# Optimization experiments

Hardware: AMD Instinct MI355X
Metric: run time of the kernel (lower is better)

## Reference

```python
import jax, jax.numpy as jnp
import numpy as np

N = 100000   # nodes
E = 1600000  # edges (avg degree 16)
D = 128      # emb_dim
L = 5        # num_layer
NUM_BOND_TYPE = 6
NUM_ATOM_TYPE = 120
EPS = 1e-5


def setup_inputs() -> dict:
    key = jax.random.key(0)
    ks = jax.random.split(key, 10)
    s = 0.05
    x = jax.random.randint(ks[0], (N, 2), 0, 3)
    edge_index = jax.random.randint(ks[1], (2, E), 0, N)
    edge_attr = jax.random.randint(ks[2], (E, 2), 0, 3)
    # learned params: x embedding table [120+3, D], per-layer edge tables [6+3, D], GIN MLPs, BN stats
    x_emb = jax.random.normal(ks[3], (123, D), dtype=jnp.float32) * s
    etab = jax.random.normal(ks[4], (L, 9, D), dtype=jnp.float32) * s
    w1 = jax.random.normal(ks[5], (L, 2 * D, D), dtype=jnp.float32) * s
    b1 = jnp.zeros((L, 2 * D), dtype=jnp.float32)
    w2 = jax.random.normal(ks[6], (L, D, 2 * D), dtype=jnp.float32) * s
    b2 = jnp.zeros((L, D), dtype=jnp.float32)
    gamma = jnp.ones((L, D), dtype=jnp.float32)
    beta = jnp.zeros((L, D), dtype=jnp.float32)
    bn_mean = jax.random.normal(ks[7], (L, D), dtype=jnp.float32) * 0.1
    bn_var = jax.random.uniform(ks[8], (L, D), minval=0.5, maxval=1.5, dtype=jnp.float32)
    return dict(x=x, edge_index=edge_index, edge_attr=edge_attr, x_emb=x_emb, etab=etab,
                w1=w1, b1=b1, w2=w2, b2=b2, gamma=gamma, beta=beta,
                bn_mean=bn_mean, bn_var=bn_var)


def reference(x, edge_index, edge_attr, x_emb, etab, w1, b1, w2, b2, gamma, beta, bn_mean, bn_var):
    # node input embedding: atom-type rows [0:120) + chirality rows [120:123)
    h = x_emb[:NUM_ATOM_TYPE][x[:, 0]] + x_emb[NUM_ATOM_TYPE:][x[:, 1]]  # [N, D]
    # add self-loops (self-loop attr = (bond_type=4, direction=0))
    loop = jnp.arange(N, dtype=edge_index.dtype)
    src = jnp.concatenate([edge_index[0], loop])  # [E+N]
    dst = jnp.concatenate([edge_index[1], loop])  # [E+N]
    eb = jnp.concatenate([edge_attr[:, 0], jnp.full((N,), 4, dtype=edge_attr.dtype)])
    ed = jnp.concatenate([edge_attr[:, 1], jnp.zeros((N,), dtype=edge_attr.dtype)])
    for l in range(L):
        # edge embedding: bond-type rows [0:6) + direction rows [6:9)
        e = etab[l][:NUM_BOND_TYPE][eb] + etab[l][NUM_BOND_TYPE:][ed]  # [E+N, D]
        msg = h[src] + e                                               # gather + add
        agg = jax.ops.segment_sum(msg, dst, num_segments=N)           # scatter-add aggregate
        # GIN MLP: Linear(D,2D) -> ReLU -> Linear(2D,D)  (torch Linear: y = x @ W.T + b)
        hmid = jax.nn.relu(jnp.einsum('nd,hd->nh', agg, w1[l]) + b1[l])
        h2 = jnp.einsum('nh,dh->nd', hmid, w2[l]) + b2[l]
        # BatchNorm1d (eval mode, running stats)
        h2 = (h2 - bn_mean[l]) * jax.lax.rsqrt(bn_var[l] + EPS) * gamma[l] + beta[l]
        h = jax.nn.relu(h2) if l < L - 1 else h2  # JK='last', dropout p=0
    return h
```

## Files before the change

kernel.cpp:

```cpp
#include <hip/hip_runtime.h>

#define D 128
#define H 256
#define NBLK 512
#define BUCKSH 8

typedef _Float16 half8 __attribute__((ext_vector_type(8)));
typedef _Float16 half4 __attribute__((ext_vector_type(4)));
typedef _Float16 half2v __attribute__((ext_vector_type(2)));
typedef float floatx4 __attribute__((ext_vector_type(4)));
typedef float floatx2 __attribute__((ext_vector_type(2)));

__device__ inline unsigned char f32_to_fp8(float v){
  int p = __builtin_amdgcn_cvt_pk_fp8_f32(v, v, 0, false);
  return (unsigned char)(p & 0xFF);
}

__global__ __launch_bounds__(256) void scan_part(const int* __restrict__ cnt,
                                                 int* __restrict__ bsum, int N){
  int base = blockIdx.x*1024;
  int tid = threadIdx.x;
  int idx = base + tid*4;
  int4 v = {0,0,0,0};
  if (idx + 3 < N) v = *(const int4*)(cnt + idx);
  else {
    if (idx   < N) v.x = cnt[idx];
    if (idx+1 < N) v.y = cnt[idx+1];
    if (idx+2 < N) v.z = cnt[idx+2];
    if (idx+3 < N) v.w = cnt[idx+3];
  }
  int s = v.x + v.y + v.z + v.w;
  #pragma unroll
  for (int off = 32; off > 0; off >>= 1) s += __shfl_down(s, off, 64);
  __shared__ int ws[4];
  int lane = tid & 63, wave = tid >> 6;
  if (lane == 0) ws[wave] = s;
  __syncthreads();
  if (tid == 0) bsum[blockIdx.x] = ws[0] + ws[1] + ws[2] + ws[3];
}

__global__ __launch_bounds__(1024) void scan_bsums(const int* __restrict__ bsum,
                                                   int* __restrict__ bbase,
                                                   int* __restrict__ total_out, int nb, int N){
  __shared__ int sh[1024];
  int tid = threadIdx.x;
  int v = (tid < nb) ? bsum[tid] : 0;
  sh[tid] = v;
  __syncthreads();
  #pragma unroll
  for (int off = 1; off < 1024; off <<= 1){
    int t = 0;
    if (tid >= off) t = sh[tid - off];
    __syncthreads();
    if (tid >= off) sh[tid] += t;
    __syncthreads();
  }
  if (tid < nb) bbase[tid] = sh[tid] - v;
  if (tid == 0) total_out[N] = sh[1023];
}

__global__ __launch_bounds__(256) void scan_emit(const int* __restrict__ cnt,
                                                 const int* __restrict__ bbase,
                                                 int* __restrict__ outp, int N){
  int base = blockIdx.x*1024;
  int tid = threadIdx.x;
  int idx = base + tid*4;
  int4 v = {0,0,0,0};
  if (idx + 3 < N) v = *(const int4*)(cnt + idx);
  else {
    if (idx   < N) v.x = cnt[idx];
    if (idx+1 < N) v.y = cnt[idx+1];
    if (idx+2 < N) v.z = cnt[idx+2];
    if (idx+3 < N) v.w = cnt[idx+3];
  }
  int s = v.x + v.y + v.z + v.w;
  int lane = tid & 63, wave = tid >> 6;
  int incl = s;
  #pragma unroll
  for (int off = 1; off < 64; off <<= 1){
    int t = __shfl_up(incl, off, 64);
    if (lane >= off) incl += t;
  }
  __shared__ int ws[4];
  if (lane == 63) ws[wave] = incl;
  __syncthreads();
  int woff = 0;
  #pragma unroll
  for (int w = 0; w < 4; ++w) if (w < wave) woff += ws[w];
  int off0 = bbase[blockIdx.x] + woff + (incl - s);
  if (idx   < N) outp[idx]   = off0;
  if (idx+1 < N) outp[idx+1] = off0 + v.x;
  if (idx+2 < N) outp[idx+2] = off0 + v.x + v.y;
  if (idx+3 < N) outp[idx+3] = off0 + v.x + v.y + v.z;
}

__global__ __launch_bounds__(256) void part_count(const int* __restrict__ dst,
                                                  int* __restrict__ cntBB,
                                                  int E, int chunk, int nbuck){
  __shared__ int lc[512];
  int b = blockIdx.x;
  for (int i = threadIdx.x; i < nbuck; i += 256) lc[i] = 0;
  __syncthreads();
  int e0 = b*chunk, e1 = min(e0 + chunk, E);
  for (int e = e0 + threadIdx.x; e < e1; e += 256)
    atomicAdd(&lc[dst[e] >> BUCKSH], 1);
  __syncthreads();
  for (int i = threadIdx.x; i < nbuck; i += 256) cntBB[i*NBLK + b] = lc[i];
}

__global__ __launch_bounds__(256) void part_bin(const int* __restrict__ src,
                                                const int* __restrict__ dst,
                                                const int* __restrict__ ea,
                                                const int* __restrict__ baseBB,
                                                unsigned* __restrict__ staged,
                                                int E, int chunk, int nbuck){
  __shared__ int run[512];
  int b = blockIdx.x;
  for (int i = threadIdx.x; i < nbuck; i += 256) run[i] = baseBB[i*NBLK + b];
  __syncthreads();
  int e0 = b*chunk, e1 = min(e0 + chunk, E);
  for (int e = e0 + threadIdx.x; e < e1; e += 256){
    int d = dst[e];
    unsigned pv = ((unsigned)(d & 255) << 24) |
                  ((unsigned)(ea[2*e]*3 + ea[2*e+1]) << 20) | (unsigned)src[e];
    int pos = atomicAdd(&run[d >> BUCKSH], 1);
    staged[pos] = pv;
  }
}

__global__ __launch_bounds__(256) void part_emit(const unsigned* __restrict__ staged,
                                                 const int* __restrict__ baseBB,
                                                 unsigned* __restrict__ packed,
                                                 int* __restrict__ rowptr,
                                                 int N, int E, int nbuck, int M){
  __shared__ int ncnt[256];
  __shared__ int sscan[256];
  __shared__ int basep[256];
  __shared__ int cur[256];
  int k = blockIdx.x;
  int tid = threadIdx.x;
  int bstart = baseBB[k*NBLK];
  int bend = (k+1 < nbuck) ? baseBB[(k+1)*NBLK] : baseBB[M];
  ncnt[tid] = 0; cur[tid] = 0;
  __syncthreads();
  for (int j = bstart + tid; j < bend; j += 256)
    atomicAdd(&ncnt[staged[j] >> 24], 1);
  __syncthreads();
  int v = ncnt[tid];
  sscan[tid] = v;
  __syncthreads();
  #pragma unroll
  for (int off = 1; off < 256; off <<= 1){
    int t = (tid >= off) ? sscan[tid-off] : 0;
    __syncthreads();
    sscan[tid] += t;
    __syncthreads();
  }
  int excl = sscan[tid] - v;
  basep[tid] = bstart + excl;
  int node = k*256 + tid;
  if (node < N) rowptr[node] = bstart + excl;
  if (k == nbuck-1 && tid == 0) rowptr[N] = E;
  __syncthreads();
  for (int j = bstart + tid; j < bend; j += 256){
    unsigned s = staged[j];
    int dloc = (int)(s >> 24);
    int pos = basep[dloc] + atomicAdd(&cur[dloc], 1);
    packed[pos] = s & 0xFFFFFFu;
  }
}

__global__ void embed_kernel(const int* __restrict__ x, const float* __restrict__ xemb,
                             unsigned char* __restrict__ h, int N){
  int t = blockIdx.x*256 + threadIdx.x;
  if (t >= N*16) return;
  int n = t >> 4, c = (t & 15) * 8;
  int x0 = x[2*n], x1 = x[2*n+1];
  const float* r0 = xemb + (size_t)x0*D + c;
  const float* r1 = xemb + (size_t)(120 + x1)*D + c;
  float f[8];
  #pragma unroll
  for (int j = 0; j < 8; ++j) f[j] = r0[j] + r1[j];
  int w0 = 0, w1v = 0;
  w0  = __builtin_amdgcn_cvt_pk_fp8_f32(f[0], f[1], w0,  false);
  w0  = __builtin_amdgcn_cvt_pk_fp8_f32(f[2], f[3], w0,  true);
  w1v = __builtin_amdgcn_cvt_pk_fp8_f32(f[4], f[5], w1v, false);
  w1v = __builtin_amdgcn_cvt_pk_fp8_f32(f[6], f[7], w1v, true);
  uint2 o; o.x = (unsigned)w0; o.y = (unsigned)w1v;
  *(uint2*)(h + (size_t)n*D + c) = o;
}

__global__ void prep_tables(const float* __restrict__ etab, const float* __restrict__ gamma,
                            const float* __restrict__ beta, const float* __restrict__ mean,
                            const float* __restrict__ var, const float* __restrict__ b2,
                            float* __restrict__ comb, float* __restrict__ sc, float* __restrict__ sh){
  int l = blockIdx.x, d = threadIdx.x;
  const float* et = etab + (size_t)l*9*D;
  float* cl = comb + (size_t)l*10*D;
  #pragma unroll
  for (int b = 0; b < 3; ++b)
    #pragma unroll
    for (int dd = 0; dd < 3; ++dd)
      cl[(b*3+dd)*D + d] = et[b*D + d] + et[(6+dd)*D + d];
  cl[9*D + d] = et[4*D + d] + et[6*D + d];
  float A = gamma[l*D+d] * rsqrtf(var[l*D+d] + 1e-5f);
  sc[l*D+d] = A;
  sh[l*D+d] = (b2[l*D+d] - mean[l*D+d]) * A + beta[l*D+d];
}

__global__ void repack_weights(const float* __restrict__ w1, const float* __restrict__ w2,
                               _Float16* __restrict__ w1f, _Float16* __restrict__ w2f, int total){
  int i = blockIdx.x*256 + threadIdx.x;
  if (i >= total) return;
  int l = i / (H*D), r = i % (H*D);
  {
    int n = r / D, k = r % D;
    w1f[(size_t)l*H*D + (size_t)(k>>3)*(H*8) + n*8 + (k&7)] = (_Float16)w1[i];
  }
  {
    int n2 = r / H, k2 = r % H;
    w2f[(size_t)l*D*H + (size_t)(k2>>3)*(D*8) + n2*8 + (k2&7)] = (_Float16)w2[i];
  }
}

__global__ __launch_bounds__(256) void agg_kernel(
    const unsigned char* __restrict__ h, const unsigned* __restrict__ packed,
    const int* __restrict__ rowptr, const float* __restrict__ comb,
    _Float16* __restrict__ agg, int N){
  __shared__ float cl[10*D];
  int tid = threadIdx.x;
  for (int i = tid; i < 10*D; i += 256) cl[i] = comb[i];
  __syncthreads();
  int lane = tid & 63;
  int q = lane >> 4, l16 = lane & 15;
  int node = blockIdx.x*16 + (tid >> 6)*4 + q;
  bool valid = node < N;
  int nd = valid ? node : 0;
  int c = l16 * 8;
  float a0, a1, a2, a3, a4, a5, a6, a7;
  {
    uint2 hx = *(const uint2*)(h + (size_t)nd*D + c);
    floatx2 s0 = __builtin_amdgcn_cvt_pk_f32_fp8((int)hx.x, false);
    floatx2 s1 = __builtin_amdgcn_cvt_pk_f32_fp8((int)hx.x, true);
    floatx2 s2 = __builtin_amdgcn_cvt_pk_f32_fp8((int)hx.y, false);
    floatx2 s3 = __builtin_amdgcn_cvt_pk_f32_fp8((int)hx.y, true);
    a0 = s0[0] + cl[9*D + c    ];
    a1 = s0[1] + cl[9*D + c + 1];
    a2 = s1[0] + cl[9*D + c + 2];
    a3 = s1[1] + cl[9*D + c + 3];
    a4 = s2[0] + cl[9*D + c + 4];
    a5 = s2[1] + cl[9*D + c + 5];
    a6 = s3[0] + cl[9*D + c + 6];
    a7 = s3[1] + cl[9*D + c + 7];
  }
  int beg = rowptr[nd], end = rowptr[nd+1];
  unsigned long long cp = 0;
  unsigned p[16], pn[16];
  {
    int m0 = end - beg;
    #pragma unroll
    for (int k = 0; k < 16; ++k) if (k < m0) p[k] = packed[beg+k];
  }
  for (int j = beg; j < end; j += 16){
    int m = end - j;
    uint2 v[16];
    #pragma unroll
    for (int k = 0; k < 16; ++k) if (k < m)
      v[k] = *(const uint2*)(h + (size_t)(p[k] & 0xFFFFFu)*D + c);
    int mn = end - (j + 16);
    #pragma unroll
    for (int k = 0; k < 16; ++k) if (k < mn) pn[k] = packed[j+16+k];
    #pragma unroll
    for (int k = 0; k < 16; ++k) if (k < m){
      cp += 1ULL << (7*(int)(p[k] >> 20));
      floatx2 g0 = __builtin_amdgcn_cvt_pk_f32_fp8((int)v[k].x, false);
      floatx2 g1 = __builtin_amdgcn_cvt_pk_f32_fp8((int)v[k].x, true);
      floatx2 g2 = __builtin_amdgcn_cvt_pk_f32_fp8((int)v[k].y, false);
      floatx2 g3 = __builtin_amdgcn_cvt_pk_f32_fp8((int)v[k].y, true);
      a0 += g0[0]; a1 += g0[1]; a2 += g1[0]; a3 += g1[1];
      a4 += g2[0]; a5 += g2[1]; a6 += g3[0]; a7 += g3[1];
    }
    #pragma unroll
    for (int k = 0; k < 16; ++k) p[k] = pn[k];
  }
  #pragma unroll
  for (int cd = 0; cd < 9; ++cd){
    float cnt = (float)(int)((cp >> (7*cd)) & 127);
    a0 += cnt * cl[cd*D + c    ];
    a1 += cnt * cl[cd*D + c + 1];
    a2 += cnt * cl[cd*D + c + 2];
    a3 += cnt * cl[cd*D + c + 3];
    a4 += cnt * cl[cd*D + c + 4];
    a5 += cnt * cl[cd*D + c + 5];
    a6 += cnt * cl[cd*D + c + 6];
    a7 += cnt * cl[cd*D + c + 7];
  }
  if (valid){
    half8 o;
    o[0] = (_Float16)a0; o[1] = (_Float16)a1;
    o[2] = (_Float16)a2; o[3] = (_Float16)a3;
    o[4] = (_Float16)a4; o[5] = (_Float16)a5;
    o[6] = (_Float16)a6; o[7] = (_Float16)a7;
    *(half8*)(agg + (size_t)node*D + c) = o;
  }
}

__global__ __launch_bounds__(256) void mlp_kernel(
    const _Float16* __restrict__ agg, const _Float16* __restrict__ w1f,
    const _Float16* __restrict__ w2f, const float* __restrict__ b1,
    const float* __restrict__ sc, const float* __restrict__ sh,
    unsigned char* __restrict__ hout, float* __restrict__ fout,
    int N, int relu_out){
  __shared__ __align__(16) char smem[64*256*2];
  _Float16* atile = (_Float16*)smem;
  _Float16* hmid  = (_Float16*)smem;
  int tid = threadIdx.x;
  int wave = tid >> 6, lane = tid & 63;
  int quad = lane >> 4, l15 = lane & 15;
  int r0 = blockIdx.x * 64;

  half8 zf;
  #pragma unroll
  for (int j = 0; j < 8; ++j) zf[j] = (_Float16)0.f;

  #pragma unroll
  for (int i = 0; i < 4; ++i){
    int ci = i*256 + tid;
    int row = ci >> 4, c8 = ci & 15;
    int m = r0 + row;
    half8 v = (m < N) ? *(const half8*)(agg + (size_t)m*D + c8*8) : zf;
    *(half8*)(atile + row*128 + ((c8 ^ (row & 15)) * 8)) = v;
  }
  __syncthreads();

  floatx4 acc[4][4] = {};
  half8 bcur[4], bnxt[4];
  #pragma unroll
  for (int nt = 0; nt < 4; ++nt)
    bcur[nt] = *(const half8*)(w1f + (size_t)quad*(H*8) + (wave*64 + nt*16 + l15)*8);
  #pragma unroll
  for (int ks = 0; ks < 4; ++ks){
    if (ks < 3){
      #pragma unroll
      for (int nt = 0; nt < 4; ++nt)
        bnxt[nt] = *(const half8*)(w1f + (size_t)((ks+1)*4 + quad)*(H*8) + (wave*64 + nt*16 + l15)*8);
    }
    int c8 = ks*4 + quad;
    half8 af[4];
    #pragma unroll
    for (int mt = 0; mt < 4; ++mt)
      af[mt] = *(const half8*)(atile + (mt*16 + l15)*128 + ((c8 ^ l15) * 8));
    #pragma unroll
    for (int mt = 0; mt < 4; ++mt)
      #pragma unroll
      for (int nt = 0; nt < 4; ++nt)
        acc[mt][nt] = __builtin_amdgcn_mfma_f32_16x16x32_f16(af[mt], bcur[nt], acc[mt][nt], 0, 0, 0);
    #pragma unroll
    for (int nt = 0; nt < 4; ++nt) bcur[nt] = bnxt[nt];
  }
  __syncthreads();

  #pragma unroll
  for (int nt = 0; nt < 4; ++nt){
    int n = wave*64 + nt*16 + l15;
    float bias = b1[n];
    #pragma unroll
    for (int mt = 0; mt < 4; ++mt)
      #pragma unroll
      for (int r = 0; r < 4; ++r){
        int row = mt*16 + quad*4 + r;
        hmid[row*256 + (((n >> 3) ^ (row & 31)) * 8) + (n & 7)] =
            (_Float16)fmaxf(acc[mt][nt][r] + bias, 0.f);
      }
  }
  __syncthreads();

  floatx4 acc2[4][2] = {};
  half8 gcur[2], gnxt[2];
  #pragma unroll
  for (int nt = 0; nt < 2; ++nt)
    gcur[nt] = *(const half8*)(w2f + (size_t)quad*(D*8) + (wave*32 + nt*16 + l15)*8);
  #pragma unroll
  for (int ks = 0; ks < 8; ++ks){
    if (ks < 7){
      #pragma unroll
      for (int nt = 0; nt < 2; ++nt)
        gnxt[nt] = *(const half8*)(w2f + (size_t)((ks+1)*4 + quad)*(D*8) + (wave*32 + nt*16 + l15)*8);
    }
    int c8 = ks*4 + quad;
    half8 af[4];
    #pragma unroll
    for (int mt = 0; mt < 4; ++mt){
      int row = mt*16 + l15;
      af[mt] = *(const half8*)(hmid + row*256 + ((c8 ^ (row & 31)) * 8));
    }
    #pragma unroll
    for (int mt = 0; mt < 4; ++mt)
      #pragma unroll
      for (int nt = 0; nt < 2; ++nt)
        acc2[mt][nt] = __builtin_amdgcn_mfma_f32_16x16x32_f16(af[mt], gcur[nt], acc2[mt][nt], 0, 0, 0);
    #pragma unroll
    for (int nt = 0; nt < 2; ++nt) gcur[nt] = gnxt[nt];
  }

  #pragma unroll
  for (int nt = 0; nt < 2; ++nt){
    int n = wave*32 + nt*16 + l15;
    float A = sc[n], B = sh[n];
    #pragma unroll
    for (int mt = 0; mt < 4; ++mt)
      #pragma unroll
      for (int r = 0; r < 4; ++r){
        int row = r0 + mt*16 + quad*4 + r;
        if (row < N){
          float v = acc2[mt][nt][r]*A + B;
          if (relu_out) v = fmaxf(v, 0.f);
          if (fout) fout[(size_t)row*D + n] = v;
          else      hout[(size_t)row*D + n] = f32_to_fp8(v);
        }
      }
  }
}

extern "C" void kernel_launch(void* const* d_in, const int* in_sizes, int n_in,
                              void* d_out, int out_size, void* d_ws, size_t ws_size,
                              hipStream_t stream){
  const int*   x     = (const int*)d_in[0];
  const int*   ei    = (const int*)d_in[1];
  const int*   ea    = (const int*)d_in[2];
  const float* xemb  = (const float*)d_in[3];
  const float* etab  = (const float*)d_in[4];
  const float* w1    = (const float*)d_in[5];
  const float* b1    = (const float*)d_in[6];
  const float* w2    = (const float*)d_in[7];
  const float* b2    = (const float*)d_in[8];
  const float* gamma = (const float*)d_in[9];
  const float* beta  = (const float*)d_in[10];
  const float* mean  = (const float*)d_in[11];
  const float* var   = (const float*)d_in[12];
  float* out = (float*)d_out;

  int N = in_sizes[0] / 2;
  int E = in_sizes[1] / 2;
  int nbuck = (N + 255) >> 8;
  int M = nbuck * NBLK;
  int nbM = (M + 1023) / 1024;
  int chunk = (E + NBLK - 1) / NBLK;

  char* ws = (char*)d_ws;
  size_t off = 0;
  auto alloc = [&](size_t b){ void* p = ws + off; off += (b + 255) & ~(size_t)255; return p; };
  unsigned char* h   = (unsigned char*)alloc((size_t)N*D);
  _Float16* agg      = (_Float16*)alloc((size_t)N*D*2);
  unsigned* packed   = (unsigned*)alloc((size_t)(E+16)*4);
  int*      rowptr   = (int*)alloc((size_t)(N+1)*4);
  int*      cntBB    = (int*)alloc((size_t)M*4);
  int*      baseBB   = (int*)alloc((size_t)(M+1)*4);
  int*      bsum     = (int*)alloc((size_t)nbM*4);
  int*      bbase    = (int*)alloc((size_t)nbM*4);
  _Float16* w1f      = (_Float16*)alloc((size_t)5*H*D*2);
  _Float16* w2f      = (_Float16*)alloc((size_t)5*D*H*2);
  float*    comb     = (float*)alloc((size_t)5*10*D*4);
  float*    sc       = (float*)alloc((size_t)5*D*4);
  float*    sh       = (float*)alloc((size_t)5*D*4);
  unsigned* staged   = (unsigned*)agg;

  const int* srcp = ei;
  const int* dstp = ei + E;

  part_count<<<NBLK, 256, 0, stream>>>(dstp, cntBB, E, chunk, nbuck);
  scan_part <<<nbM, 256, 0, stream>>>(cntBB, bsum, M);
  scan_bsums<<<1, 1024, 0, stream>>>(bsum, bbase, baseBB, nbM, M);
  scan_emit <<<nbM, 256, 0, stream>>>(cntBB, bbase, baseBB, M);
  part_bin  <<<NBLK, 256, 0, stream>>>(srcp, dstp, ea, baseBB, staged, E, chunk, nbuck);
  part_emit <<<nbuck, 256, 0, stream>>>(staged, baseBB, packed, rowptr, N, E, nbuck, M);
  repack_weights<<<(5*H*D+255)/256, 256, 0, stream>>>(w1, w2, w1f, w2f, 5*H*D);
  prep_tables<<<5, 128, 0, stream>>>(etab, gamma, beta, mean, var, b2, comb, sc, sh);
  embed_kernel<<<((size_t)N*16+255)/256, 256, 0, stream>>>(x, xemb, h, N);

  for (int l = 0; l < 5; ++l){
    agg_kernel<<<(N+15)/16, 256, 0, stream>>>(h, packed, rowptr, comb + (size_t)l*10*D, agg, N);
    int last = (l == 4);
    mlp_kernel<<<(N+63)/64, 256, 0, stream>>>(agg, w1f + (size_t)l*H*D, w2f + (size_t)l*D*H,
        b1 + (size_t)l*H, sc + (size_t)l*D, sh + (size_t)l*D,
        last ? (unsigned char*)nullptr : h, last ? out : (float*)nullptr,
        N, last ? 0 : 1);
  }
}
```

Baseline: 577.2 us.

## Precompute per-node edge-code counts and double-buffer neighbor gathers in aggregation

```diff
diff --git a/kernel.cpp b/kernel.cpp
--- a/kernel.cpp
+++ b/kernel.cpp
@@ -170,6 +170,18 @@
   }
 }
 
+__global__ __launch_bounds__(256) void code_counts(const unsigned* __restrict__ packed,
+                                                   const int* __restrict__ rowptr,
+                                                   unsigned long long* __restrict__ cpt, int N){
+  int n = blockIdx.x*256 + threadIdx.x;
+  if (n >= N) return;
+  int b = rowptr[n], e = rowptr[n+1];
+  unsigned long long cp = 0;
+  for (int j = b; j < e; ++j)
+    cp += 1ULL << (7*(int)(packed[j] >> 20));
+  cpt[n] = cp;
+}
+
 __global__ void embed_kernel(const int* __restrict__ x, const float* __restrict__ xemb,
                              unsigned char* __restrict__ h, int N){
   int t = blockIdx.x*256 + threadIdx.x;
@@ -225,8 +237,8 @@
 
 __global__ __launch_bounds__(256) void agg_kernel(
     const unsigned char* __restrict__ h, const unsigned* __restrict__ packed,
-    const int* __restrict__ rowptr, const float* __restrict__ comb,
-    _Float16* __restrict__ agg, int N){
+    const int* __restrict__ rowptr, const unsigned long long* __restrict__ cpt,
+    const float* __restrict__ comb, _Float16* __restrict__ agg, int N){
   __shared__ float cl[10*D];
   int tid = threadIdx.x;
   for (int i = tid; i < 10*D; i += 256) cl[i] = comb[i];
@@ -254,34 +266,52 @@
     a7 = s3[1] + cl[9*D + c + 7];
   }
   int beg = rowptr[nd], end = rowptr[nd+1];
-  unsigned long long cp = 0;
-  unsigned p[16], pn[16];
+  unsigned long long cp = cpt[nd];
+
+  unsigned iA[16], iB[16];
+  uint2 gA[16], gB[16];
   {
     int m0 = end - beg;
     #pragma unroll
-    for (int k = 0; k < 16; ++k) if (k < m0) p[k] = packed[beg+k];
-  }
-  for (int j = beg; j < end; j += 16){
-    int m = end - j;
-    uint2 v[16];
-    #pragma unroll
-    for (int k = 0; k < 16; ++k) if (k < m)
-      v[k] = *(const uint2*)(h + (size_t)(p[k] & 0xFFFFFu)*D + c);
-    int mn = end - (j + 16);
-    #pragma unroll
-    for (int k = 0; k < 16; ++k) if (k < mn) pn[k] = packed[j+16+k];
-    #pragma unroll
-    for (int k = 0; k < 16; ++k) if (k < m){
-      cp += 1ULL << (7*(int)(p[k] >> 20));
-      floatx2 g0 = __builtin_amdgcn_cvt_pk_f32_fp8((int)v[k].x, false);
-      floatx2 g1 = __builtin_amdgcn_cvt_pk_f32_fp8((int)v[k].x, true);
-      floatx2 g2 = __builtin_amdgcn_cvt_pk_f32_fp8((int)v[k].y, false);
-      floatx2 g3 = __builtin_amdgcn_cvt_pk_f32_fp8((int)v[k].y, true);
+    for (int k = 0; k < 16; ++k) if (k < m0) iA[k] = packed[beg+k];
+    #pragma unroll
+    for (int k = 0; k < 16; ++k) if (k < m0)
+      gA[k] = *(const uint2*)(h + (size_t)(iA[k] & 0xFFFFFu)*D + c);
+    int m1 = m0 - 16;
+    #pragma unroll
+    for (int k = 0; k < 16; ++k) if (k < m1) iB[k] = packed[beg+16+k];
+  }
+  for (int j = beg; j < end; j += 32){
+    int m0 = end - j, m1 = m0 - 16, m2 = m0 - 32, m3 = m0 - 48;
+    #pragma unroll
+    for (int k = 0; k < 16; ++k) if (k < m1)
+      gB[k] = *(const uint2*)(h + (size_t)(iB[k] & 0xFFFFFu)*D + c);
+    #pragma unroll
+    for (int k = 0; k < 16; ++k) if (k < m2) iA[k] = packed[j+32+k];
+    #pragma unroll
+    for (int k = 0; k < 16; ++k) if (k < m0){
+      floatx2 g0 = __builtin_amdgcn_cvt_pk_f32_fp8((int)gA[k].x, false);
+      floatx2 g1 = __builtin_amdgcn_cvt_pk_f32_fp8((int)gA[k].x, true);
+      floatx2 g2 = __builtin_amdgcn_cvt_pk_f32_fp8((int)gA[k].y, false);
+      floatx2 g3 = __builtin_amdgcn_cvt_pk_f32_fp8((int)gA[k].y, true);
       a0 += g0[0]; a1 += g0[1]; a2 += g1[0]; a3 += g1[1];
       a4 += g2[0]; a5 += g2[1]; a6 += g3[0]; a7 += g3[1];
     }
-    #pragma unroll
-    for (int k = 0; k < 16; ++k) p[k] = pn[k];
+    if (m1 <= 0) break;
+    #pragma unroll
+    for (int k = 0; k < 16; ++k) if (k < m2)
+      gA[k] = *(const uint2*)(h + (size_t)(iA[k] & 0xFFFFFu)*D + c);
+    #pragma unroll
+    for (int k = 0; k < 16; ++k) if (k < m3) iB[k] = packed[j+48+k];
+    #pragma unroll
+    for (int k = 0; k < 16; ++k) if (k < m1){
+      floatx2 g0 = __builtin_amdgcn_cvt_pk_f32_fp8((int)gB[k].x, false);
+      floatx2 g1 = __builtin_amdgcn_cvt_pk_f32_fp8((int)gB[k].x, true);
+      floatx2 g2 = __builtin_amdgcn_cvt_pk_f32_fp8((int)gB[k].y, false);
+      floatx2 g3 = __builtin_amdgcn_cvt_pk_f32_fp8((int)gB[k].y, true);
+      a0 += g0[0]; a1 += g0[1]; a2 += g1[0]; a3 += g1[1];
+      a4 += g2[0]; a5 += g2[1]; a6 += g3[0]; a7 += g3[1];
+    }
   }
   #pragma unroll
   for (int cd = 0; cd < 9; ++cd){
@@ -452,8 +482,9 @@
   auto alloc = [&](size_t b){ void* p = ws + off; off += (b + 255) & ~(size_t)255; return p; };
   unsigned char* h   = (unsigned char*)alloc((size_t)N*D);
   _Float16* agg      = (_Float16*)alloc((size_t)N*D*2);
-  unsigned* packed   = (unsigned*)alloc((size_t)(E+16)*4);
+  unsigned* packed   = (unsigned*)alloc((size_t)(E+64)*4);
   int*      rowptr   = (int*)alloc((size_t)(N+1)*4);
+  unsigned long long* cpt = (unsigned long long*)alloc((size_t)N*8);
   int*      cntBB    = (int*)alloc((size_t)M*4);
   int*      baseBB   = (int*)alloc((size_t)(M+1)*4);
   int*      bsum     = (int*)alloc((size_t)nbM*4);
@@ -474,12 +505,14 @@
   scan_emit <<<nbM, 256, 0, stream>>>(cntBB, bbase, baseBB, M);
   part_bin  <<<NBLK, 256, 0, stream>>>(srcp, dstp, ea, baseBB, staged, E, chunk, nbuck);
   part_emit <<<nbuck, 256, 0, stream>>>(staged, baseBB, packed, rowptr, N, E, nbuck, M);
+  code_counts<<<(N+255)/256, 256, 0, stream>>>(packed, rowptr, cpt, N);
   repack_weights<<<(5*H*D+255)/256, 256, 0, stream>>>(w1, w2, w1f, w2f, 5*H*D);
   prep_tables<<<5, 128, 0, stream>>>(etab, gamma, beta, mean, var, b2, comb, sc, sh);
   embed_kernel<<<((size_t)N*16+255)/256, 256, 0, stream>>>(x, xemb, h, N);
 
   for (int l = 0; l < 5; ++l){
-    agg_kernel<<<(N+15)/16, 256, 0, stream>>>(h, packed, rowptr, comb + (size_t)l*10*D, agg, N);
+    agg_kernel<<<(N+15)/16, 256, 0, stream>>>(h, packed, rowptr, cpt,
+        comb + (size_t)l*10*D, agg, N);
     int last = (l == 4);
     mlp_kernel<<<(N+63)/64, 256, 0, stream>>>(agg, w1f + (size_t)l*H*D, w2f + (size_t)l*D*H,
         b1 + (size_t)l*H, sc + (size_t)l*D, sh + (size_t)l*D,
```

Result: slower. 909.7 us (+57.6%).

## Fuse neighbor aggregation into GIN MLP kernel with ping-pong feature buffers

Applied to the files above, without the earlier changes.

```diff
diff --git a/kernel.cpp b/kernel.cpp
--- a/kernel.cpp
+++ b/kernel.cpp
@@ -7,7 +7,6 @@
 
 typedef _Float16 half8 __attribute__((ext_vector_type(8)));
 typedef _Float16 half4 __attribute__((ext_vector_type(4)));
-typedef _Float16 half2v __attribute__((ext_vector_type(2)));
 typedef float floatx4 __attribute__((ext_vector_type(4)));
 typedef float floatx2 __attribute__((ext_vector_type(2)));
 
@@ -223,113 +222,97 @@
   }
 }
 
-__global__ __launch_bounds__(256) void agg_kernel(
-    const unsigned char* __restrict__ h, const unsigned* __restrict__ packed,
+__global__ __launch_bounds__(256) void gin_fused(
+    const unsigned char* __restrict__ hin, const unsigned* __restrict__ packed,
     const int* __restrict__ rowptr, const float* __restrict__ comb,
-    _Float16* __restrict__ agg, int N){
-  __shared__ float cl[10*D];
+    const _Float16* __restrict__ w1f, const _Float16* __restrict__ w2f,
+    const float* __restrict__ b1, const float* __restrict__ sc,
+    const float* __restrict__ sh, unsigned char* __restrict__ hout,
+    float* __restrict__ fout, int N, int relu_out){
+  __shared__ __align__(16) char smem[64*256*2 + 10*128*4];
+  _Float16* atile = (_Float16*)smem;
+  _Float16* hmid  = (_Float16*)smem;
+  float* cl = (float*)(smem + 64*256*2);
   int tid = threadIdx.x;
+  int wave = tid >> 6, lane = tid & 63;
+  int quad = lane >> 4, l15 = lane & 15;
+  int r0 = blockIdx.x * 64;
+
   for (int i = tid; i < 10*D; i += 256) cl[i] = comb[i];
   __syncthreads();
-  int lane = tid & 63;
+
   int q = lane >> 4, l16 = lane & 15;
-  int node = blockIdx.x*16 + (tid >> 6)*4 + q;
-  bool valid = node < N;
-  int nd = valid ? node : 0;
   int c = l16 * 8;
-  float a0, a1, a2, a3, a4, a5, a6, a7;
-  {
-    uint2 hx = *(const uint2*)(h + (size_t)nd*D + c);
-    floatx2 s0 = __builtin_amdgcn_cvt_pk_f32_fp8((int)hx.x, false);
-    floatx2 s1 = __builtin_amdgcn_cvt_pk_f32_fp8((int)hx.x, true);
-    floatx2 s2 = __builtin_amdgcn_cvt_pk_f32_fp8((int)hx.y, false);
-    floatx2 s3 = __builtin_amdgcn_cvt_pk_f32_fp8((int)hx.y, true);
-    a0 = s0[0] + cl[9*D + c    ];
-    a1 = s0[1] + cl[9*D + c + 1];
-    a2 = s1[0] + cl[9*D + c + 2];
-    a3 = s1[1] + cl[9*D + c + 3];
-    a4 = s2[0] + cl[9*D + c + 4];
-    a5 = s2[1] + cl[9*D + c + 5];
-    a6 = s3[0] + cl[9*D + c + 6];
-    a7 = s3[1] + cl[9*D + c + 7];
-  }
-  int beg = rowptr[nd], end = rowptr[nd+1];
-  unsigned long long cp = 0;
-  unsigned p[16], pn[16];
-  {
-    int m0 = end - beg;
-    #pragma unroll
-    for (int k = 0; k < 16; ++k) if (k < m0) p[k] = packed[beg+k];
-  }
-  for (int j = beg; j < end; j += 16){
-    int m = end - j;
-    uint2 v[16];
-    #pragma unroll
-    for (int k = 0; k < 16; ++k) if (k < m)
-      v[k] = *(const uint2*)(h + (size_t)(p[k] & 0xFFFFFu)*D + c);
-    int mn = end - (j + 16);
-    #pragma unroll
-    for (int k = 0; k < 16; ++k) if (k < mn) pn[k] = packed[j+16+k];
-    #pragma unroll
-    for (int k = 0; k < 16; ++k) if (k < m){
-      cp += 1ULL << (7*(int)(p[k] >> 20));
-      floatx2 g0 = __builtin_amdgcn_cvt_pk_f32_fp8((int)v[k].x, false);
-      floatx2 g1 = __builtin_amdgcn_cvt_pk_f32_fp8((int)v[k].x, true);
-      floatx2 g2 = __builtin_amdgcn_cvt_pk_f32_fp8((int)v[k].y, false);
-      floatx2 g3 = __builtin_amdgcn_cvt_pk_f32_fp8((int)v[k].y, true);
-      a0 += g0[0]; a1 += g0[1]; a2 += g1[0]; a3 += g1[1];
-      a4 += g2[0]; a5 += g2[1]; a6 += g3[0]; a7 += g3[1];
-    }
-    #pragma unroll
-    for (int k = 0; k < 16; ++k) p[k] = pn[k];
-  }
-  #pragma unroll
-  for (int cd = 0; cd < 9; ++cd){
-    float cnt = (float)(int)((cp >> (7*cd)) & 127);
-    a0 += cnt * cl[cd*D + c    ];
-    a1 += cnt * cl[cd*D + c + 1];
-    a2 += cnt * cl[cd*D + c + 2];
-    a3 += cnt * cl[cd*D + c + 3];
-    a4 += cnt * cl[cd*D + c + 4];
-    a5 += cnt * cl[cd*D + c + 5];
-    a6 += cnt * cl[cd*D + c + 6];
-    a7 += cnt * cl[cd*D + c + 7];
-  }
-  if (valid){
+  #pragma unroll 1
+  for (int it = 0; it < 4; ++it){
+    int row = wave*16 + it*4 + q;
+    int node = r0 + row;
+    bool valid = node < N;
+    int nd = valid ? node : 0;
+    float a0, a1, a2, a3, a4, a5, a6, a7;
+    {
+      uint2 hx = *(const uint2*)(hin + (size_t)nd*D + c);
+      floatx2 s0 = __builtin_amdgcn_cvt_pk_f32_fp8((int)hx.x, false);
+      floatx2 s1 = __builtin_amdgcn_cvt_pk_f32_fp8((int)hx.x, true);
+      floatx2 s2 = __builtin_amdgcn_cvt_pk_f32_fp8((int)hx.y, false);
+      floatx2 s3 = __builtin_amdgcn_cvt_pk_f32_fp8((int)hx.y, true);
+      a0 = s0[0] + cl[9*D + c    ];
+      a1 = s0[1] + cl[9*D + c + 1];
+      a2 = s1[0] + cl[9*D + c + 2];
+      a3 = s1[1] + cl[9*D + c + 3];
+      a4 = s2[0] + cl[9*D + c + 4];
+      a5 = s2[1] + cl[9*D + c + 5];
+      a6 = s3[0] + cl[9*D + c + 6];
+      a7 = s3[1] + cl[9*D + c + 7];
+    }
+    int beg = rowptr[nd], end = rowptr[nd+1];
+    unsigned long long cp = 0;
+    unsigned p[16], pn[16];
+    {
+      int m0 = end - beg;
+      #pragma unroll
+      for (int k = 0; k < 16; ++k) if (k < m0) p[k] = packed[beg+k];
+    }
+    for (int j = beg; j < end; j += 16){
+      int m = end - j;
+      uint2 v[16];
+      #pragma unroll
+      for (int k = 0; k < 16; ++k) if (k < m)
+        v[k] = *(const uint2*)(hin + (size_t)(p[k] & 0xFFFFFu)*D + c);
+      int mn = end - (j + 16);
+      #pragma unroll
+      for (int k = 0; k < 16; ++k) if (k < mn) pn[k] = packed[j+16+k];
+      #pragma unroll
+      for (int k = 0; k < 16; ++k) if (k < m){
+        cp += 1ULL << (7*(int)(p[k] >> 20));
+        floatx2 g0 = __builtin_amdgcn_cvt_pk_f32_fp8((int)v[k].x, false);
+        floatx2 g1 = __builtin_amdgcn_cvt_pk_f32_fp8((int)v[k].x, true);
+        floatx2 g2 = __builtin_amdgcn_cvt_pk_f32_fp8((int)v[k].y, false);
+        floatx2 g3 = __builtin_amdgcn_cvt_pk_f32_fp8((int)v[k].y, true);
+        a0 += g0[0]; a1 += g0[1]; a2 += g1[0]; a3 += g1[1];
+        a4 += g2[0]; a5 += g2[1]; a6 += g3[0]; a7 += g3[1];
+      }
+      #pragma unroll
+      for (int k = 0; k < 16; ++k) p[k] = pn[k];
+    }
+    #pragma unroll
+    for (int cd = 0; cd < 9; ++cd){
+      float cnt = (float)(int)((cp >> (7*cd)) & 127);
+      a0 += cnt * cl[cd*D + c    ];
+      a1 += cnt * cl[cd*D + c + 1];
+      a2 += cnt * cl[cd*D + c + 2];
+      a3 += cnt * cl[cd*D + c + 3];
+      a4 += cnt * cl[cd*D + c + 4];
+      a5 += cnt * cl[cd*D + c + 5];
+      a6 += cnt * cl[cd*D + c + 6];
+      a7 += cnt * cl[cd*D + c + 7];
+    }
     half8 o;
     o[0] = (_Float16)a0; o[1] = (_Float16)a1;
     o[2] = (_Float16)a2; o[3] = (_Float16)a3;
     o[4] = (_Float16)a4; o[5] = (_Float16)a5;
     o[6] = (_Float16)a6; o[7] = (_Float16)a7;
-    *(half8*)(agg + (size_t)node*D + c) = o;
-  }
-}
-
-__global__ __launch_bounds__(256) void mlp_kernel(
-    const _Float16* __restrict__ agg, const _Float16* __restrict__ w1f,
-    const _Float16* __restrict__ w2f, const float* __restrict__ b1,
-    const float* __restrict__ sc, const float* __restrict__ sh,
-    unsigned char* __restrict__ hout, float* __restrict__ fout,
-    int N, int relu_out){
-  __shared__ __align__(16) char smem[64*256*2];
-  _Float16* atile = (_Float16*)smem;
-  _Float16* hmid  = (_Float16*)smem;
-  int tid = threadIdx.x;
-  int wave = tid >> 6, lane = tid & 63;
-  int quad = lane >> 4, l15 = lane & 15;
-  int r0 = blockIdx.x * 64;
-
-  half8 zf;
-  #pragma unroll
-  for (int j = 0; j < 8; ++j) zf[j] = (_Float16)0.f;
-
-  #pragma unroll
-  for (int i = 0; i < 4; ++i){
-    int ci = i*256 + tid;
-    int row = ci >> 4, c8 = ci & 15;
-    int m = r0 + row;
-    half8 v = (m < N) ? *(const half8*)(agg + (size_t)m*D + c8*8) : zf;
-    *(half8*)(atile + row*128 + ((c8 ^ (row & 15)) * 8)) = v;
+    *(half8*)(atile + row*128 + ((l16 ^ (row & 15)) * 8)) = o;
   }
   __syncthreads();
 
@@ -450,9 +433,9 @@
   char* ws = (char*)d_ws;
   size_t off = 0;
   auto alloc = [&](size_t b){ void* p = ws + off; off += (b + 255) & ~(size_t)255; return p; };
-  unsigned char* h   = (unsigned char*)alloc((size_t)N*D);
-  _Float16* agg      = (_Float16*)alloc((size_t)N*D*2);
-  unsigned* packed   = (unsigned*)alloc((size_t)(E+16)*4);
+  unsigned char* ha  = (unsigned char*)alloc((size_t)N*D);
+  unsigned char* hb  = (unsigned char*)alloc((size_t)N*D);
+  unsigned* packed   = (unsigned*)alloc((size_t)(E+64)*4);
   int*      rowptr   = (int*)alloc((size_t)(N+1)*4);
   int*      cntBB    = (int*)alloc((size_t)M*4);
   int*      baseBB   = (int*)alloc((size_t)(M+1)*4);
@@ -463,7 +446,7 @@
   float*    comb     = (float*)alloc((size_t)5*10*D*4);
   float*    sc       = (float*)alloc((size_t)5*D*4);
   float*    sh       = (float*)alloc((size_t)5*D*4);
-  unsigned* staged   = (unsigned*)agg;
+  unsigned* staged   = (unsigned*)hb;
 
   const int* srcp = ei;
   const int* dstp = ei + E;
@@ -476,14 +459,17 @@
   part_emit <<<nbuck, 256, 0, stream>>>(staged, baseBB, packed, rowptr, N, E, nbuck, M);
   repack_weights<<<(5*H*D+255)/256, 256, 0, stream>>>(w1, w2, w1f, w2f, 5*H*D);
   prep_tables<<<5, 128, 0, stream>>>(etab, gamma, beta, mean, var, b2, comb, sc, sh);
-  embed_kernel<<<((size_t)N*16+255)/256, 256, 0, stream>>>(x, xemb, h, N);
-
+  embed_kernel<<<((size_t)N*16+255)/256, 256, 0, stream>>>(x, xemb, ha, N);
+
+  const unsigned char* hin = ha;
+  unsigned char* hob = hb;
   for (int l = 0; l < 5; ++l){
-    agg_kernel<<<(N+15)/16, 256, 0, stream>>>(h, packed, rowptr, comb + (size_t)l*10*D, agg, N);
     int last = (l == 4);
-    mlp_kernel<<<(N+63)/64, 256, 0, stream>>>(agg, w1f + (size_t)l*H*D, w2f + (size_t)l*D*H,
+    gin_fused<<<(N+63)/64, 256, 0, stream>>>(hin, packed, rowptr,
+        comb + (size_t)l*10*D, w1f + (size_t)l*H*D, w2f + (size_t)l*D*H,
         b1 + (size_t)l*H, sc + (size_t)l*D, sh + (size_t)l*D,
-        last ? (unsigned char*)nullptr : h, last ? out : (float*)nullptr,
+        last ? (unsigned char*)nullptr : hob, last ? out : (float*)nullptr,
         N, last ? 0 : 1);
-  }
-}
+    unsigned char* t = (unsigned char*)hin; hin = hob; hob = t;
+  }
+}
```

Result: slower. 711.0 us (+23.2%).
